# Kernel tuning notes

Hardware: AMD Instinct MI355X
Metric: run time of the kernel (lower is better)

Reference implementation:

```python
import jax, jax.numpy as jnp
import numpy as np

STRIDE = (2, 2)
PADDING = ((1, 1), (1, 1))


def setup_inputs() -> dict:
    key = jax.random.key(0)
    k1, k2, k3, k4 = jax.random.split(key, 4)
    B, Cin, H, W = 32, 128, 112, 112
    Cout, E, kh, kw = 256, 4, 3, 3
    x = jax.random.normal(k1, (B, Cin, H, W), dtype=jnp.float32)
    routing_w = jax.random.normal(k2, (E, Cin), dtype=jnp.float32) * (1.0 / np.sqrt(Cin))
    routing_b = jax.random.normal(k3, (E,), dtype=jnp.float32) * 0.01
    expert_weight = jax.random.normal(k4, (E, Cout, Cin, kh, kw), dtype=jnp.float32) * (1.0 / np.sqrt(Cin * kh * kw))
    return {"x": x, "routing_w": routing_w, "routing_b": routing_b, "expert_weight": expert_weight}


def reference(x, routing_w, routing_b, expert_weight):
    # Routing: global average pool -> linear -> sigmoid  (B, E)
    pooled = jnp.mean(x, axis=(2, 3))
    rw = jax.nn.sigmoid(pooled @ routing_w.T + routing_b)
    # Per-sample dynamic kernels: (B, Cout, Cin, kh, kw)
    kernels = jnp.einsum('be,eoihw->boihw', rw, expert_weight)

    def conv_one(xi, wi):
        # xi: (Cin, H, W), wi: (Cout, Cin, kh, kw)
        return jax.lax.conv_general_dilated(
            xi[None], wi, window_strides=STRIDE, padding=PADDING,
            dimension_numbers=('NCHW', 'OIHW', 'NCHW'))[0]

    return jax.vmap(conv_one)(x, kernels)
```

## Files before the change

### kernel.cpp

```cpp
#include <hip/hip_runtime.h>
#include <cstdint>

typedef unsigned short u16;
typedef unsigned int u32;

typedef __attribute__((ext_vector_type(8))) short bf16x8;
typedef __attribute__((ext_vector_type(4))) float f32x4;

#define KDIM 1152
#define MDIM 256
#define NPIX 3136
#define PLANE 12544
#define EWSTRIDE 294912
#define HH 114
#define XT_SAMP ((size_t)HH * HH * 128)

__device__ __forceinline__ u16 f2bf(float f) {
  u32 u = __float_as_uint(f);
  return (u16)((u + 0x7FFFu + ((u >> 16) & 1u)) >> 16);
}

__device__ __forceinline__ void gl_lds16(const u16* g, u16* l) {
  __builtin_amdgcn_global_load_lds((__attribute__((address_space(1))) void*)g,
                                   (__attribute__((address_space(3))) void*)l,
                                   16, 0, 0);
}

__global__ __launch_bounds__(256) void transpose_pool_kernel(
    const float* __restrict__ x, u16* __restrict__ xt, float* __restrict__ part) {
  __shared__ u32 tile[112 * 68];
  __shared__ float psum[512];
  const int h = blockIdx.x, b = blockIdx.y;
  const int t = threadIdx.x, lane = t & 63, wave = t >> 6;

  {
    u32* xrow = (u32*)xt + ((size_t)b * HH + (h + 1)) * HH * 64;
    if (t < 128) {
      const int w = (t >= 64) ? 113 : 0;
      xrow[(size_t)w * 64 + (t & 63)] = 0u;
    }
    if (h == 0 || h == 111) {
      u32* xr = (u32*)xt + ((size_t)b * HH + (h == 0 ? 0 : 113)) * HH * 64;
      for (int i = t; i < HH * 64; i += 256) xr[i] = 0u;
    }
  }

  const float* xb = x + (size_t)b * 128 * PLANE + h * 112;
  if (lane < 56) {
    #pragma unroll
    for (int wh = 0; wh < 2; ++wh) {
      const int w = wh * 56 + lane;
      #pragma unroll
      for (int i = 0; i < 4; ++i) {
        const int ci0 = (i * 4 + wave) * 8;
        const float* p = xb + (size_t)ci0 * PLANE + w;
        float v0 = p[0];
        float v1 = p[(size_t)1 * PLANE];
        float v2 = p[(size_t)2 * PLANE];
        float v3 = p[(size_t)3 * PLANE];
        float v4 = p[(size_t)4 * PLANE];
        float v5 = p[(size_t)5 * PLANE];
        float v6 = p[(size_t)6 * PLANE];
        float v7 = p[(size_t)7 * PLANE];
        uint4 d;
        d.x = (u32)f2bf(v0) | ((u32)f2bf(v1) << 16);
        d.y = (u32)f2bf(v2) | ((u32)f2bf(v3) << 16);
        d.z = (u32)f2bf(v4) | ((u32)f2bf(v5) << 16);
        d.w = (u32)f2bf(v6) | ((u32)f2bf(v7) << 16);
        *(uint4*)&tile[w * 68 + ci0 / 2] = d;
      }
    }
  }
  __syncthreads();
  const int c = t & 63;
  float s0 = 0.f, s1 = 0.f;
  u32* xg = (u32*)xt + (((size_t)b * HH + h + 1) * HH + 1) * 64;
  #pragma unroll
  for (int j = 0; j < 28; ++j) {
    const int idx = t + 256 * j;
    const int w = idx >> 6;
    const u32 v = tile[w * 68 + c];
    s0 += __uint_as_float(v << 16);
    s1 += __uint_as_float(v & 0xffff0000u);
    xg[(size_t)w * 64 + c] = v;
  }
  psum[wave * 128 + 2 * c] = s0;
  psum[wave * 128 + 2 * c + 1] = s1;
  __syncthreads();
  if (t < 128)
    part[((size_t)h * 32 + b) * 128 + t] =
        psum[t] + psum[128 + t] + psum[256 + t] + psum[384 + t];
}

__global__ __launch_bounds__(256) void reduce_routing_kernel(
    const float* __restrict__ part, const float* __restrict__ rww,
    const float* __restrict__ rwb, float* __restrict__ rw) {
  __shared__ float red[256];
  __shared__ float pl[128];
  const int b = blockIdx.x, t = threadIdx.x;
  const int ci = t & 127, half = t >> 7;
  float s = 0.f;
  const float* p = part + ((size_t)(half * 56) * 32 + b) * 128 + ci;
  #pragma unroll 4
  for (int h = 0; h < 56; ++h) s += p[(size_t)h * 32 * 128];
  red[t] = s;
  __syncthreads();
  if (t < 128) pl[t] = red[t] + red[t + 128];
  __syncthreads();
  const int e = t >> 6, l = t & 63;
  float acc = pl[l] * rww[e * 128 + l] + pl[l + 64] * rww[e * 128 + l + 64];
  #pragma unroll
  for (int off = 32; off > 0; off >>= 1) acc += __shfl_down(acc, off, 64);
  if (l == 0) {
    const float logit = acc * (1.0f / (float)PLANE) + rwb[e];
    rw[b * 4 + e] = 1.0f / (1.0f + expf(-logit));
  }
}

__global__ __launch_bounds__(256) void mix_kernel(const float* __restrict__ ew,
                                                  const float* __restrict__ rw,
                                                  u16* __restrict__ wmix) {
  const int t = threadIdx.x;
  const int oc = blockIdx.x * 4 + (t >> 6);
  const int lane = t & 63;
  const int b0 = blockIdx.y * 4;
  float ereg[4][18];
  #pragma unroll
  for (int e = 0; e < 4; ++e) {
    const float* p = ew + ((size_t)e * 256 + oc) * 1152 + lane * 18;
    #pragma unroll
    for (int j = 0; j < 18; ++j) ereg[e][j] = p[j];
  }
  for (int bb = 0; bb < 4; ++bb) {
    const int b = b0 + bb;
    const float w0 = rw[b * 4 + 0], w1 = rw[b * 4 + 1];
    const float w2 = rw[b * 4 + 2], w3 = rw[b * 4 + 3];
    u32* dst = (u32*)(wmix + ((size_t)b * 256 + oc) * KDIM) + lane;
    #pragma unroll
    for (int r = 0; r < 9; ++r) {
      const float va = w0 * ereg[0][r] + w1 * ereg[1][r] + w2 * ereg[2][r] + w3 * ereg[3][r];
      const float vb = w0 * ereg[0][9 + r] + w1 * ereg[1][9 + r] + w2 * ereg[2][9 + r] + w3 * ereg[3][9 + r];
      dst[r * 64] = (u32)f2bf(va) | ((u32)f2bf(vb) << 16);
    }
  }
}

__global__ __launch_bounds__(256) void gemm_kernel(const u16* __restrict__ wmix,
                                                   const u16* __restrict__ xt,
                                                   float* __restrict__ out) {
  __shared__ u16 a_sm[2][128 * 32];
  __shared__ u16 b_sm[2][128 * 32];
  const int b = blockIdx.x;
  const int mt = blockIdx.y & 1, nt = blockIdx.y >> 1;
  const int tid = threadIdx.x, lane = tid & 63, wave = tid >> 6;
  const int srow = lane >> 2, scol = (lane & 3) * 8;
  const u16* ga0 = wmix + (size_t)b * EWSTRIDE + (size_t)(mt * 128 + wave * 16 + srow) * KDIM + scol;
  const u16* ga1 = ga0 + 64 * KDIM;
  const u16* xtb = xt + (size_t)b * XT_SAMP;
  int p0 = nt * 128 + wave * 16 + (lane >> 2);
  int p1 = p0 + 64;
  if (p0 > NPIX - 1) p0 = NPIX - 1;
  if (p1 > NPIX - 1) p1 = NPIX - 1;
  const size_t pb0 = ((size_t)(2 * (p0 / 56)) * HH + 2 * (p0 % 56)) * 128 + scol;
  const size_t pb1 = ((size_t)(2 * (p1 / 56)) * HH + 2 * (p1 % 56)) * 128 + scol;

  u16* la00 = &a_sm[0][wave * 512 + lane * 8];
  u16* la01 = la00 + 2048;
  u16* la10 = &a_sm[1][wave * 512 + lane * 8];
  u16* la11 = la10 + 2048;
  u16* lb00 = &b_sm[0][wave * 512 + lane * 8];
  u16* lb01 = lb00 + 2048;
  u16* lb10 = &b_sm[1][wave * 512 + lane * 8];
  u16* lb11 = lb10 + 2048;

  const int wm = wave >> 1, wn = wave & 1;
  const int fr = lane & 15, quad = lane >> 4;
  f32x4 acc[4][4];
  const f32x4 zv = {0.f, 0.f, 0.f, 0.f};
  #pragma unroll
  for (int i = 0; i < 4; ++i)
    #pragma unroll
    for (int j = 0; j < 4; ++j) acc[i][j] = zv;

  for (int kt2 = 0; kt2 < 18; ++kt2) {
    const int k0 = kt2 * 2;
    const int r = k0 >> 2;
    const size_t tap = (size_t)((r / 3) * HH + (r % 3)) * 128;
    const size_t t0 = tap + (size_t)(k0 & 3) * 32;
    const size_t t1 = t0 + 32;
    gl_lds16(ga0 + k0 * 32, la00);
    gl_lds16(ga1 + k0 * 32, la01);
    gl_lds16(xtb + pb0 + t0, lb00);
    gl_lds16(xtb + pb1 + t0, lb01);
    gl_lds16(ga0 + k0 * 32 + 32, la10);
    gl_lds16(ga1 + k0 * 32 + 32, la11);
    gl_lds16(xtb + pb0 + t1, lb10);
    gl_lds16(xtb + pb1 + t1, lb11);
    __syncthreads();
    #pragma unroll
    for (int c = 0; c < 2; ++c) {
      const u16* as = a_sm[c];
      const u16* bs = b_sm[c];
      bf16x8 av[4], bv[4];
      #pragma unroll
      for (int i = 0; i < 4; ++i)
        av[i] = *(const bf16x8*)(as + (wm * 64 + i * 16 + fr) * 32 + quad * 8);
      #pragma unroll
      for (int j = 0; j < 4; ++j)
        bv[j] = *(const bf16x8*)(bs + (wn * 64 + j * 16 + fr) * 32 + quad * 8);
      #pragma unroll
      for (int i = 0; i < 4; ++i)
        #pragma unroll
        for (int j = 0; j < 4; ++j)
          acc[i][j] = __builtin_amdgcn_mfma_f32_16x16x32_bf16(av[i], bv[j], acc[i][j], 0, 0, 0);
    }
    __syncthreads();
  }

  float* os = out + (size_t)b * MDIM * NPIX;
  const int mbase = mt * 128 + wm * 64 + quad * 4;
  const int nb = nt * 128 + wn * 64 + fr;
  #pragma unroll
  for (int j = 0; j < 4; ++j) {
    const int n = nb + j * 16;
    if (n < NPIX) {
      #pragma unroll
      for (int i = 0; i < 4; ++i) {
        const int m = mbase + i * 16;
        #pragma unroll
        for (int rr = 0; rr < 4; ++rr)
          os[(size_t)(m + rr) * NPIX + n] = acc[i][j][rr];
      }
    }
  }
}

__global__ void routing_kernel(const float* __restrict__ pooled,
                               const float* __restrict__ rww,
                               const float* __restrict__ rwb,
                               float* __restrict__ rw, float scale) {
  const int t = threadIdx.x;
  if (t >= 128) return;
  const int b = t >> 2, e = t & 3;
  float acc = rwb[e];
  for (int c = 0; c < 128; ++c) acc += pooled[b * 128 + c] * scale * rww[e * 128 + c];
  rw[b * 4 + e] = 1.0f / (1.0f + expf(-acc));
}

__global__ __launch_bounds__(256) void pool_kernel(const float* __restrict__ x,
                                                   float* __restrict__ pooled) {
  const int ci = blockIdx.x, b = blockIdx.y;
  const float4* p = (const float4*)(x + ((size_t)b * 128 + ci) * PLANE);
  float s = 0.f;
  for (int i = threadIdx.x; i < PLANE / 4; i += 256) {
    float4 v = p[i];
    s += v.x + v.y + v.z + v.w;
  }
  #pragma unroll
  for (int off = 32; off > 0; off >>= 1) s += __shfl_down(s, off, 64);
  __shared__ float red[4];
  if ((threadIdx.x & 63) == 0) red[threadIdx.x >> 6] = s;
  __syncthreads();
  if (threadIdx.x == 0)
    pooled[b * 128 + ci] = (red[0] + red[1] + red[2] + red[3]) * (1.0f / (float)PLANE);
}

__global__ __launch_bounds__(256) void naive_conv(const float* __restrict__ x,
                                                  const float* __restrict__ ew,
                                                  const float* __restrict__ rw,
                                                  float* __restrict__ out) {
  const size_t idx = (size_t)blockIdx.x * 256 + threadIdx.x;
  if (idx >= (size_t)32 * MDIM * NPIX) return;
  const int n = (int)(idx % NPIX);
  const int tmp = (int)(idx / NPIX);
  const int oc = tmp % MDIM;
  const int b = tmp / MDIM;
  const int oh = n / 56, ow = n % 56;
  const float w0 = rw[b * 4 + 0], w1 = rw[b * 4 + 1];
  const float w2 = rw[b * 4 + 2], w3 = rw[b * 4 + 3];
  float acc = 0.f;
  for (int ci = 0; ci < 128; ++ci) {
    const float* xp = x + ((size_t)b * 128 + ci) * PLANE;
    const size_t wb = ((size_t)oc * 128 + ci) * 9;
    for (int kh = 0; kh < 3; ++kh) {
      const int ih = 2 * oh - 1 + kh;
      if (ih < 0 || ih >= 112) continue;
      for (int kw = 0; kw < 3; ++kw) {
        const int iw = 2 * ow - 1 + kw;
        if (iw < 0 || iw >= 112) continue;
        const int ko = kh * 3 + kw;
        const float wsum = w0 * ew[wb + ko] + w1 * ew[(size_t)EWSTRIDE + wb + ko]
                         + w2 * ew[2 * (size_t)EWSTRIDE + wb + ko]
                         + w3 * ew[3 * (size_t)EWSTRIDE + wb + ko];
        acc += xp[ih * 112 + iw] * wsum;
      }
    }
  }
  out[idx] = acc;
}

extern "C" void kernel_launch(void* const* d_in, const int* in_sizes, int n_in,
                              void* d_out, int out_size, void* d_ws, size_t ws_size,
                              hipStream_t stream) {
  const float* x   = (const float*)d_in[0];
  const float* rww = (const float*)d_in[1];
  const float* rwb = (const float*)d_in[2];
  const float* ew  = (const float*)d_in[3];
  float* out = (float*)d_out;

  const size_t xt_bytes = 32 * XT_SAMP * 2;
  const size_t wmix_off = xt_bytes;
  const size_t part_off = wmix_off + (size_t)32 * EWSTRIDE * 2;
  const size_t pooled_off = part_off + (size_t)112 * 32 * 128 * 4;
  const size_t rw_off = pooled_off + 16384;
  const size_t need = rw_off + 512;

  if (ws_size >= need) {
    u16* xt = (u16*)d_ws;
    u16* wmix = (u16*)((char*)d_ws + wmix_off);
    float* part = (float*)((char*)d_ws + part_off);
    float* rw_ws = (float*)((char*)d_ws + rw_off);
    transpose_pool_kernel<<<dim3(112, 32), 256, 0, stream>>>(x, xt, part);
    reduce_routing_kernel<<<32, 256, 0, stream>>>(part, rww, rwb, rw_ws);
    mix_kernel<<<dim3(64, 8), 256, 0, stream>>>(ew, rw_ws, wmix);
    gemm_kernel<<<dim3(32, 50), 256, 0, stream>>>(wmix, xt, out);
  } else {
    float* pooled = (float*)d_ws;
    float* rw_ws = (float*)((char*)d_ws + 16384);
    pool_kernel<<<dim3(128, 32), 256, 0, stream>>>(x, pooled);
    routing_kernel<<<1, 128, 0, stream>>>(pooled, rww, rwb, rw_ws, 1.0f);
    naive_conv<<<(int)(((size_t)32 * MDIM * NPIX + 255) / 256), 256, 0, stream>>>(
        x, ew, rw_ws, out);
  }
}
```

Baseline: 443.4 us.

## Double-buffer GEMM LDS stages and vectorize input transpose loads

The GEMM main loop now uses two LDS buffers, issuing global-to-LDS loads for the next K step while MFMAs run on the current one. This hides load latency behind compute, at the cost of doubling shared memory to 64 KB per block, which may lower occupancy. Separately, the prep kernel reads two adjacent width elements per float2 load and writes two transposed tile rows, halving the number of global load instructions.

```diff
diff --git a/kernel.cpp b/kernel.cpp
--- a/kernel.cpp
+++ b/kernel.cpp
@@ -47,28 +47,30 @@
 
   const float* xb = x + (size_t)b * 128 * PLANE + h * 112;
   if (lane < 56) {
+    const int w0 = 2 * lane;
     #pragma unroll
-    for (int wh = 0; wh < 2; ++wh) {
-      const int w = wh * 56 + lane;
-      #pragma unroll
-      for (int i = 0; i < 4; ++i) {
-        const int ci0 = (i * 4 + wave) * 8;
-        const float* p = xb + (size_t)ci0 * PLANE + w;
-        float v0 = p[0];
-        float v1 = p[(size_t)1 * PLANE];
-        float v2 = p[(size_t)2 * PLANE];
-        float v3 = p[(size_t)3 * PLANE];
-        float v4 = p[(size_t)4 * PLANE];
-        float v5 = p[(size_t)5 * PLANE];
-        float v6 = p[(size_t)6 * PLANE];
-        float v7 = p[(size_t)7 * PLANE];
-        uint4 d;
-        d.x = (u32)f2bf(v0) | ((u32)f2bf(v1) << 16);
-        d.y = (u32)f2bf(v2) | ((u32)f2bf(v3) << 16);
-        d.z = (u32)f2bf(v4) | ((u32)f2bf(v5) << 16);
-        d.w = (u32)f2bf(v6) | ((u32)f2bf(v7) << 16);
-        *(uint4*)&tile[w * 68 + ci0 / 2] = d;
-      }
+    for (int i = 0; i < 4; ++i) {
+      const int ci0 = (i * 4 + wave) * 8;
+      const float* p = xb + (size_t)ci0 * PLANE + w0;
+      float2 q0 = *(const float2*)(p);
+      float2 q1 = *(const float2*)(p + (size_t)1 * PLANE);
+      float2 q2 = *(const float2*)(p + (size_t)2 * PLANE);
+      float2 q3 = *(const float2*)(p + (size_t)3 * PLANE);
+      float2 q4 = *(const float2*)(p + (size_t)4 * PLANE);
+      float2 q5 = *(const float2*)(p + (size_t)5 * PLANE);
+      float2 q6 = *(const float2*)(p + (size_t)6 * PLANE);
+      float2 q7 = *(const float2*)(p + (size_t)7 * PLANE);
+      uint4 dE, dO;
+      dE.x = (u32)f2bf(q0.x) | ((u32)f2bf(q1.x) << 16);
+      dO.x = (u32)f2bf(q0.y) | ((u32)f2bf(q1.y) << 16);
+      dE.y = (u32)f2bf(q2.x) | ((u32)f2bf(q3.x) << 16);
+      dO.y = (u32)f2bf(q2.y) | ((u32)f2bf(q3.y) << 16);
+      dE.z = (u32)f2bf(q4.x) | ((u32)f2bf(q5.x) << 16);
+      dO.z = (u32)f2bf(q4.y) | ((u32)f2bf(q5.y) << 16);
+      dE.w = (u32)f2bf(q6.x) | ((u32)f2bf(q7.x) << 16);
+      dO.w = (u32)f2bf(q6.y) | ((u32)f2bf(q7.y) << 16);
+      *(uint4*)&tile[(size_t)w0 * 68 + ci0 / 2] = dE;
+      *(uint4*)&tile[(size_t)(w0 + 1) * 68 + ci0 / 2] = dO;
     }
   }
   __syncthreads();
@@ -148,8 +150,8 @@
 __global__ __launch_bounds__(256) void gemm_kernel(const u16* __restrict__ wmix,
                                                    const u16* __restrict__ xt,
                                                    float* __restrict__ out) {
-  __shared__ u16 a_sm[2][128 * 32];
-  __shared__ u16 b_sm[2][128 * 32];
+  __shared__ u16 a_sm[2][2][128 * 32];
+  __shared__ u16 b_sm[2][2][128 * 32];
   const int b = blockIdx.x;
   const int mt = blockIdx.y & 1, nt = blockIdx.y >> 1;
   const int tid = threadIdx.x, lane = tid & 63, wave = tid >> 6;
@@ -164,14 +166,8 @@
   const size_t pb0 = ((size_t)(2 * (p0 / 56)) * HH + 2 * (p0 % 56)) * 128 + scol;
   const size_t pb1 = ((size_t)(2 * (p1 / 56)) * HH + 2 * (p1 % 56)) * 128 + scol;
 
-  u16* la00 = &a_sm[0][wave * 512 + lane * 8];
-  u16* la01 = la00 + 2048;
-  u16* la10 = &a_sm[1][wave * 512 + lane * 8];
-  u16* la11 = la10 + 2048;
-  u16* lb00 = &b_sm[0][wave * 512 + lane * 8];
-  u16* lb01 = lb00 + 2048;
-  u16* lb10 = &b_sm[1][wave * 512 + lane * 8];
-  u16* lb11 = lb10 + 2048;
+  u16* const la = &a_sm[0][0][wave * 512 + lane * 8];
+  u16* const lb = &b_sm[0][0][wave * 512 + lane * 8];
 
   const int wm = wave >> 1, wn = wave & 1;
   const int fr = lane & 15, quad = lane >> 4;
@@ -182,40 +178,65 @@
     #pragma unroll
     for (int j = 0; j < 4; ++j) acc[i][j] = zv;
 
-  for (int kt2 = 0; kt2 < 18; ++kt2) {
-    const int k0 = kt2 * 2;
-    const int r = k0 >> 2;
-    const size_t tap = (size_t)((r / 3) * HH + (r % 3)) * 128;
-    const size_t t0 = tap + (size_t)(k0 & 3) * 32;
-    const size_t t1 = t0 + 32;
-    gl_lds16(ga0 + k0 * 32, la00);
-    gl_lds16(ga1 + k0 * 32, la01);
-    gl_lds16(xtb + pb0 + t0, lb00);
-    gl_lds16(xtb + pb1 + t0, lb01);
-    gl_lds16(ga0 + k0 * 32 + 32, la10);
-    gl_lds16(ga1 + k0 * 32 + 32, la11);
-    gl_lds16(xtb + pb0 + t1, lb10);
-    gl_lds16(xtb + pb1 + t1, lb11);
+#define STAGE(S, KT) do {                                                      \
+    const int k0_ = (KT) * 2;                                                  \
+    const int r_ = k0_ >> 2;                                                   \
+    const size_t tp_ = (size_t)((r_ / 3) * HH + (r_ % 3)) * 128                \
+                     + (size_t)(k0_ & 3) * 32;                                 \
+    const u16* a0_ = ga0 + k0_ * 32;                                           \
+    const u16* a1_ = ga1 + k0_ * 32;                                           \
+    const u16* b0_ = xtb + pb0 + tp_;                                          \
+    const u16* b1_ = xtb + pb1 + tp_;                                          \
+    u16* la_ = la + (S) * 8192;                                                \
+    u16* lb_ = lb + (S) * 8192;                                                \
+    gl_lds16(a0_, la_);                                                        \
+    gl_lds16(a1_, la_ + 2048);                                                 \
+    gl_lds16(a0_ + 32, la_ + 4096);                                            \
+    gl_lds16(a1_ + 32, la_ + 6144);                                            \
+    gl_lds16(b0_, lb_);                                                        \
+    gl_lds16(b1_, lb_ + 2048);                                                 \
+    gl_lds16(b0_ + 32, lb_ + 4096);                                            \
+    gl_lds16(b1_ + 32, lb_ + 6144);                                            \
+  } while (0)
+
+#define COMPUTE(S) do {                                                        \
+    _Pragma("unroll")                                                          \
+    for (int c_ = 0; c_ < 2; ++c_) {                                           \
+      const u16* as_ = &a_sm[S][c_][0];                                        \
+      const u16* bs_ = &b_sm[S][c_][0];                                        \
+      bf16x8 av[4], bv[4];                                                     \
+      _Pragma("unroll")                                                        \
+      for (int i = 0; i < 4; ++i)                                              \
+        av[i] = *(const bf16x8*)(as_ + (wm * 64 + i * 16 + fr) * 32 + quad * 8);\
+      _Pragma("unroll")                                                        \
+      for (int j = 0; j < 4; ++j)                                              \
+        bv[j] = *(const bf16x8*)(bs_ + (wn * 64 + j * 16 + fr) * 32 + quad * 8);\
+      _Pragma("unroll")                                                        \
+      for (int i = 0; i < 4; ++i)                                              \
+        _Pragma("unroll")                                                      \
+        for (int j = 0; j < 4; ++j)                                            \
+          acc[i][j] = __builtin_amdgcn_mfma_f32_16x16x32_bf16(av[i], bv[j],    \
+                                                              acc[i][j], 0, 0, 0);\
+    }                                                                          \
+  } while (0)
+
+  STAGE(0, 0);
+  __syncthreads();
+  for (int i = 0; i < 8; ++i) {
+    STAGE(1, 2 * i + 1);
+    COMPUTE(0);
     __syncthreads();
-    #pragma unroll
-    for (int c = 0; c < 2; ++c) {
-      const u16* as = a_sm[c];
-      const u16* bs = b_sm[c];
-      bf16x8 av[4], bv[4];
-      #pragma unroll
-      for (int i = 0; i < 4; ++i)
-        av[i] = *(const bf16x8*)(as + (wm * 64 + i * 16 + fr) * 32 + quad * 8);
-      #pragma unroll
-      for (int j = 0; j < 4; ++j)
-        bv[j] = *(const bf16x8*)(bs + (wn * 64 + j * 16 + fr) * 32 + quad * 8);
-      #pragma unroll
-      for (int i = 0; i < 4; ++i)
-        #pragma unroll
-        for (int j = 0; j < 4; ++j)
-          acc[i][j] = __builtin_amdgcn_mfma_f32_16x16x32_bf16(av[i], bv[j], acc[i][j], 0, 0, 0);
-    }
+    STAGE(0, 2 * i + 2);
+    COMPUTE(1);
     __syncthreads();
   }
+  STAGE(1, 17);
+  COMPUTE(0);
+  __syncthreads();
+  COMPUTE(1);
+
+#undef STAGE
+#undef COMPUTE
 
   float* os = out + (size_t)b * MDIM * NPIX;
   const int mbase = mt * 128 + wm * 64 + quad * 4;
```

New measurement: 444.9 us. No clear change (+0.3%).
